# Kernel tuning notes

Measured on AMD Instinct MI355X. Metric: run time of the kernel, lower is better.

## Reference

```python
import jax, jax.numpy as jnp
import numpy as np

NUM_HEADS = 8
WINDOW = 7
DILATION = 1
EPS = 1e-5


def channel_ln(x, w, b):
    # x: [B, C, H, W]; normalize over channel dim (axis=1)
    mu = jnp.mean(x, axis=1, keepdims=True)
    var = jnp.var(x, axis=1, keepdims=True)
    xhat = (x - mu) * jax.lax.rsqrt(var + EPS)
    return xhat * w[None, :, None, None] + b[None, :, None, None]


def local_mask(H, W, window, dilation):
    r = (window // 2) * dilation
    ii, jj = jnp.meshgrid(jnp.arange(H), jnp.arange(W), indexing="ij")
    ii = ii.reshape(-1)
    jj = jj.reshape(-1)
    di = jnp.abs(ii[:, None] - ii[None, :])
    dj = jnp.abs(jj[:, None] - jj[None, :])
    m = (di <= r) & (dj <= r)
    if dilation > 1:
        m = m & (di % dilation == 0) & (dj % dilation == 0)
    return m  # [N, N] bool


def local_attention(x, qkv_w, qkv_b, proj_w, proj_b):
    B, C, H, W = x.shape
    N = H * W
    hd = C // NUM_HEADS
    t = x.reshape(B, C, N).transpose(0, 2, 1)            # [B, N, C]
    qkv = t @ qkv_w.T + qkv_b                            # [B, N, 3C]
    qkv = qkv.reshape(B, N, 3, NUM_HEADS, hd)
    q, k, v = (qkv[:, :, i].transpose(0, 2, 1, 3) for i in range(3))  # [B,h,N,d]
    scale = 1.0 / jnp.sqrt(jnp.asarray(hd, x.dtype))
    scores = jnp.einsum("bhnd,bhmd->bhnm", q, k) * scale  # [B,h,N,N]
    mask = local_mask(H, W, WINDOW, DILATION)             # [N,N]
    scores = jnp.where(mask[None, None], scores, jnp.asarray(-jnp.inf, x.dtype))
    attn = jax.nn.softmax(scores, axis=-1)
    out = jnp.einsum("bhnm,bhmd->bhnd", attn, v)          # [B,h,N,d]
    out = out.transpose(0, 2, 1, 3).reshape(B, N, C)      # [B,N,C]
    out = out @ proj_w.T + proj_b
    return out.transpose(0, 2, 1).reshape(B, C, H, W)


def mlp2d(x, fc1_w, fc1_b, fc2_w, fc2_b):
    # 1x1 convs == per-pixel linear over channels
    h = jnp.einsum("bchw,oc->bohw", x, fc1_w) + fc1_b[None, :, None, None]
    h = jax.nn.gelu(h, approximate=False)
    return jnp.einsum("bchw,oc->bohw", h, fc2_w) + fc2_b[None, :, None, None]


def setup_inputs() -> dict:
    key = jax.random.key(0)
    ks = jax.random.split(key, 12)
    B, C, H, W = 1, 256, 56, 56
    hidden = 4 * C
    s = lambda fan: 1.0 / np.sqrt(fan)
    return {
        "x": jax.random.normal(ks[0], (B, C, H, W), jnp.float32),
        "norm1_w": jnp.ones((C,), jnp.float32),
        "norm1_b": jnp.zeros((C,), jnp.float32),
        "qkv_w": jax.random.normal(ks[1], (3 * C, C), jnp.float32) * s(C),
        "qkv_b": jnp.zeros((3 * C,), jnp.float32),
        "proj_w": jax.random.normal(ks[2], (C, C), jnp.float32) * s(C),
        "proj_b": jnp.zeros((C,), jnp.float32),
        "norm2_w": jnp.ones((C,), jnp.float32),
        "norm2_b": jnp.zeros((C,), jnp.float32),
        "fc1_w": jax.random.normal(ks[3], (hidden, C), jnp.float32) * s(C),
        "fc1_b": jnp.zeros((hidden,), jnp.float32),
        "fc2_w": jax.random.normal(ks[4], (C, hidden), jnp.float32) * s(hidden),
        "fc2_b": jnp.zeros((C,), jnp.float32),
    }


def reference(x, norm1_w, norm1_b, qkv_w, qkv_b, proj_w, proj_b,
              norm2_w, norm2_b, fc1_w, fc1_b, fc2_w, fc2_b):
    x = x + local_attention(channel_ln(x, norm1_w, norm1_b), qkv_w, qkv_b, proj_w, proj_b)
    x = x + mlp2d(channel_ln(x, norm2_w, norm2_b), fc1_w, fc1_b, fc2_w, fc2_b)
    return x
```

## Files before the change

kernel.cpp:

```cpp
#include <hip/hip_runtime.h>
#include <math.h>


typedef unsigned int uint;
typedef unsigned short ushort;
typedef unsigned long long u64;
typedef __attribute__((ext_vector_type(8))) short short8;
typedef __attribute__((ext_vector_type(4))) float floatx4;
typedef __attribute__((ext_vector_type(4))) unsigned short ushort4v;

#define AS1(p) (const __attribute__((address_space(1))) void*)(p)
#define AS3(p) (__attribute__((address_space(3))) void*)(p)

__device__ __forceinline__ float bf2f(ushort u) {
  union { uint i; float f; } v; v.i = ((uint)u) << 16; return v.f;
}
__device__ __forceinline__ ushort f2bf(float f) {
  union { float f; uint i; } v; v.f = f;
  uint u = v.i;
  return (ushort)((u + 0x7fffu + ((u >> 16) & 1u)) >> 16);
}

__device__ __forceinline__ void stage64(const ushort* src, int kstride,
                                        ushort* dstBase, int tid) {
  const int srow = tid >> 5;
  const int scb  = (tid & 31) ^ srow;
  const ushort* g = src + (size_t)srow * kstride + scb * 8;
  ushort* d = dstBase + tid * 8;
  #pragma unroll
  for (int r = 0; r < 8; ++r) {
    __builtin_amdgcn_global_load_lds(AS1(g), AS3(d), 16, 0, 0);
    g += 8 * kstride;
    d += 2048;
  }
}

__device__ __forceinline__ void compute64(const ushort* As, const ushort* Bs,
                                          int w, int lane, floatx4 acc[4]) {
  const int fm = lane & 15;
  const int q  = lane >> 4;
  const int swz = fm & 7;
  const int arow = (w * 16 + fm) * 256;
  #pragma unroll
  for (int kt = 0; kt < 8; ++kt) {
    const int blk = ((kt * 4 + q) ^ swz) * 8;
    short8 af = *(const short8*)&As[arow + blk];
    #pragma unroll
    for (int nt = 0; nt < 4; ++nt) {
      short8 bfr = *(const short8*)&Bs[(nt * 16 + fm) * 256 + blk];
      acc[nt] = __builtin_amdgcn_mfma_f32_16x16x32_bf16(af, bfr, acc[nt], 0, 0, 0);
    }
  }
}

__global__ __launch_bounds__(256) void prep_kernel(
    const float* __restrict__ x, const float* __restrict__ n1w,
    const float* __restrict__ n1b, const float* __restrict__ qkvw,
    ushort* __restrict__ t1, ushort* __restrict__ wcat)
{
  const int tid = threadIdx.x;
  const int bid = blockIdx.x;
  if (bid >= 196) {
    int idx = (bid - 196) * 256 + tid;
    wcat[idx] = f2bf(qkvw[idx]);
    return;
  }
  __shared__ float tile[256 * 17];
  __shared__ float red[2][16][16];
  __shared__ float mu[16], rsv[16];
  const int n0 = bid * 16;
  const int px = tid & 15, grp = tid >> 4;
  #pragma unroll 4
  for (int it = 0; it < 16; ++it) {
    int c = it * 16 + grp;
    tile[c * 17 + px] = x[(size_t)c * 3136 + n0 + px];
  }
  __syncthreads();
  float s = 0.f, ss = 0.f;
  #pragma unroll
  for (int i = 0; i < 16; ++i) {
    float v = tile[(grp * 16 + i) * 17 + px];
    s += v; ss += v * v;
  }
  red[0][px][grp] = s; red[1][px][grp] = ss;
  __syncthreads();
  if (tid < 16) {
    float s2 = 0.f, ss2 = 0.f;
    #pragma unroll
    for (int g = 0; g < 16; ++g) { s2 += red[0][tid][g]; ss2 += red[1][tid][g]; }
    float m = s2 * (1.f / 256.f);
    float var = ss2 * (1.f / 256.f) - m * m;
    mu[tid] = m;
    rsv[tid] = rsqrtf(var + 1e-5f);
  }
  __syncthreads();
  const float wc = n1w[tid], bc = n1b[tid];
  #pragma unroll 4
  for (int p = 0; p < 16; ++p) {
    float v = tile[tid * 17 + p];
    t1[(size_t)(n0 + p) * 256 + tid] = f2bf((v - mu[p]) * rsv[p] * wc + bc);
  }
}

__global__ __launch_bounds__(256, 2) void qkv_kernel(
    const ushort* __restrict__ A, const ushort* __restrict__ B,
    const float* __restrict__ bias, ushort* __restrict__ out,
    const float* __restrict__ projw, const float* __restrict__ f1w,
    const float* __restrict__ f2w, ushort* __restrict__ wcat)
{
  const int tid = threadIdx.x;
  if (blockIdx.y >= 49) {
    int c = (blockIdx.y - 49) * 12 + blockIdx.x;
    int idx = c * 256 + tid;
    float v;
    if (idx < 65536)        v = projw[idx];
    else if (idx < 327680)  v = f1w[idx - 65536];
    else                    v = f2w[idx - 327680];
    wcat[196608 + idx] = f2bf(v);
    return;
  }
  __shared__ ushort As[16384], Bs[16384];
  const int lane = tid & 63, w = tid >> 6;
  const int m0 = blockIdx.y * 64, n0 = blockIdx.x * 64;
  floatx4 acc[4] = {{0.f,0.f,0.f,0.f},{0.f,0.f,0.f,0.f},
                    {0.f,0.f,0.f,0.f},{0.f,0.f,0.f,0.f}};
  stage64(A + (size_t)m0 * 256, 256, As, tid);
  stage64(B + (size_t)n0 * 256, 256, Bs, tid);
  asm volatile("s_waitcnt vmcnt(0)" ::: "memory");
  __syncthreads();
  compute64(As, Bs, w, lane, acc);
  const int fm = lane & 15, q4 = (lane >> 4) * 4;
  #pragma unroll
  for (int nt = 0; nt < 4; ++nt)
    #pragma unroll
    for (int r = 0; r < 4; ++r) {
      int m = m0 + w * 16 + q4 + r;
      int n = n0 + nt * 16 + fm;
      float v = acc[nt][r] + bias[n];
      if (n < 256) v *= 0.17677669529663687f;
      out[(size_t)m * 768 + n] = f2bf(v);
    }
}

#define AM_SMEM 145952

__global__ __launch_bounds__(512, 1) void attnmlp_kernel(
    const ushort* __restrict__ qkv, const ushort* __restrict__ pw_bf,
    const float* __restrict__ projb, const float* __restrict__ x,
    const ushort* __restrict__ f1_bf, const float* __restrict__ f1b,
    const ushort* __restrict__ f2_bf, const float* __restrict__ f2b,
    const float* __restrict__ n2w, const float* __restrict__ n2b,
    float* __restrict__ outf)
{
  __shared__ __align__(16) char smem[AM_SMEM];
  ushort* Kh    = (ushort*)smem;
  ushort* Vh    = (ushort*)(smem + 52000);
  float*  pr    = (float*)(smem + 103200);
  ushort* aas   = (ushort*)(smem + 137504);
  ushort* pslab = (ushort*)smem;
  float*  x1s   = (float*)(smem + 103200);
  ushort* hbuf  = (ushort*)smem;
  ushort* fslab = (ushort*)(smem + 32768);
  ushort* t2s   = (ushort*)(smem + 120096);
  float*  pstat = (float*)(smem + 128288);
  float*  stats = (float*)(smem + 129312);

  const int tid = threadIdx.x;
  const int wv = tid >> 6, lane = tid & 63;
  const int fm = lane & 15, q = lane >> 4;
  const int l4 = lane >> 2, lb = lane & 3;
  const int i0 = (blockIdx.x / 14) * 4, j0 = (blockIdx.x % 14) * 4;

  for (int s = tid; s < 3200; s += 512) {
    int p = s >> 5, ck = s & 31;
    int ii = i0 - 3 + p / 10, jj = j0 - 3 + p % 10;
    if (ii >= 0 && ii < 56 && jj >= 0 && jj < 56) {
      const ushort* kr = qkv + (size_t)(ii * 56 + jj) * 768 + 256 + ck * 8;
      short8 kv = *(const short8*)kr;
      u64 lo = ((const u64*)&kv)[0], hi = ((const u64*)&kv)[1];
      *(u64*)&Kh[p * 260 + ck * 8] = lo;
      *(u64*)&Kh[p * 260 + ck * 8 + 4] = hi;
      *(short8*)&Vh[p * 256 + ck * 8] = *(const short8*)(kr + 256);
    } else {
      *(u64*)&Kh[p * 260 + ck * 8] = 0ull;
      *(u64*)&Kh[p * 260 + ck * 8 + 4] = 0ull;
      short8 z = {0, 0, 0, 0, 0, 0, 0, 0};
      *(short8*)&Vh[p * 256 + ck * 8] = z;
    }
  }
  __syncthreads();

  {
    const int h = lane >> 3, mg = lane & 7;
    #pragma unroll
    for (int qq = 0; qq < 2; ++qq) {
      const int p = wv * 2 + qq;
      const int qi = p >> 2, qj = p & 3;
      const int iq = i0 + qi, jq = j0 + qj;
      const ushort* qp = qkv + (size_t)(iq * 56 + jq) * 768 + h * 32;
      float qf[32];
      #pragma unroll
      for (int u = 0; u < 4; ++u) {
        short8 qv = *(const short8*)(qp + u * 8);
        #pragma unroll
        for (int e = 0; e < 8; ++e) qf[u * 8 + e] = bf2f((ushort)qv[e]);
      }
      float sv[7];
      float mx = -1e30f;
      #pragma unroll
      for (int k = 0; k < 7; ++k) {
        int m = mg + 8 * k;
        float s = -1e30f;
        if (m < 49) {
          int mi = m / 7, mj = m % 7;
          int ii = iq + mi - 3, jj = jq + mj - 3;
          if (ii >= 0 && ii < 56 && jj >= 0 && jj < 56) {
            int hrow = (qi + mi) * 10 + (qj + mj);
            const u64* k8 = (const u64*)&Kh[hrow * 260 + h * 32];
            float a = 0.f;
            #pragma unroll
            for (int u = 0; u < 8; ++u) {
              u64 kv = k8[u];
              #pragma unroll
              for (int e = 0; e < 4; ++e)
                a += qf[u * 4 + e] * bf2f((ushort)(kv >> (16 * e)));
            }
            s = a;
          }
        }
        sv[k] = s;
        mx = fmaxf(mx, s);
      }
      mx = fmaxf(mx, __shfl_xor(mx, 1));
      mx = fmaxf(mx, __shfl_xor(mx, 2));
      mx = fmaxf(mx, __shfl_xor(mx, 4));
      float sm = 0.f;
      #pragma unroll
      for (int k = 0; k < 7; ++k) { sv[k] = __expf(sv[k] - mx); sm += sv[k]; }
      sm += __shfl_xor(sm, 1);
      sm += __shfl_xor(sm, 2);
      sm += __shfl_xor(sm, 4);
      float inv = 1.f / sm;
      #pragma unroll
      for (int k = 0; k < 7; ++k) {
        int m = mg + 8 * k;
        pr[(p * 8 + h) * 67 + m] = sv[k] * inv;
      }
    }
  }
  __syncthreads();

  ushort* ps0 = pslab + wv * 2048;
  ushort* ps1 = ps0 + 1024;
#define STAGE_P(kt, buf) do { \
    _Pragma("unroll") \
    for (int i_ = 0; i_ < 2; ++i_) { \
      int row_ = i_ * 16 + l4; \
      const ushort* g_ = pw_bf + (size_t)(wv * 32 + row_) * 256 + (kt) * 32 + (lb ^ (row_ & 3)) * 8; \
      __builtin_amdgcn_global_load_lds(AS1(g_), AS3((buf) + i_ * 512 + lane * 8), 16, 0, 0); \
    } } while (0)
  STAGE_P(0, ps0);

  {
    const int p = tid >> 5, cg = tid & 31, hh = cg >> 2;
    const int qi = p >> 2, qj = p & 3;
    float acc8[8] = {0, 0, 0, 0, 0, 0, 0, 0};
    #pragma unroll
    for (int mi = 0; mi < 7; ++mi)
      #pragma unroll
      for (int mj = 0; mj < 7; ++mj) {
        int m = mi * 7 + mj;
        int hrow = (qi + mi) * 10 + (qj + mj);
        float pm = pr[(p * 8 + hh) * 67 + m];
        short8 v8 = *(const short8*)&Vh[hrow * 256 + cg * 8];
        #pragma unroll
        for (int e = 0; e < 8; ++e)
          acc8[e] += pm * bf2f((ushort)v8[e]);
      }
    short8 o;
    #pragma unroll
    for (int e = 0; e < 8; ++e) o[e] = (short)f2bf(acc8[e]);
    *(short8*)&aas[p * 264 + cg * 8] = o;
  }
  __syncthreads();

  {
    floatx4 pacc[2] = {{0.f,0.f,0.f,0.f},{0.f,0.f,0.f,0.f}};
    for (int kt = 0; kt < 8; ++kt) {
      ushort* cur = (kt & 1) ? ps1 : ps0;
      ushort* nxt = (kt & 1) ? ps0 : ps1;
      if (kt < 7) {
        STAGE_P(kt + 1, nxt);
        asm volatile("s_waitcnt vmcnt(2)" ::: "memory");
      } else {
        asm volatile("s_waitcnt vmcnt(0)" ::: "memory");
      }
      short8 af = *(const short8*)&aas[fm * 264 + kt * 32 + q * 8];
      #pragma unroll
      for (int nt = 0; nt < 2; ++nt) {
        int r = nt * 16 + fm;
        short8 bfr = *(const short8*)&cur[r * 32 + (q ^ (r & 3)) * 8];
        pacc[nt] = __builtin_amdgcn_mfma_f32_16x16x32_bf16(af, bfr, pacc[nt], 0, 0, 0);
      }
    }
    #pragma unroll
    for (int nt = 0; nt < 2; ++nt) {
      int ch = wv * 32 + nt * 16 + fm;
      floatx4 rx = *(const floatx4*)(x + (size_t)ch * 3136 + (i0 + q) * 56 + j0);
      #pragma unroll
      for (int r = 0; r < 4; ++r) {
        int px = q * 4 + r;
        x1s[px * 264 + ch] = pacc[nt][r] + projb[ch] + rx[r];
      }
    }
  }
  ushort* fs0 = fslab + wv * 4096;
  ushort* fs1 = fs0 + 2048;
#define STAGE_F1(c, kt, buf) do { \
    _Pragma("unroll") \
    for (int i_ = 0; i_ < 4; ++i_) { \
      int row_ = i_ * 16 + l4; \
      const ushort* g_ = f1_bf + (size_t)((c) * 64 + row_) * 256 + (kt) * 32 + (lb ^ (row_ & 3)) * 8; \
      __builtin_amdgcn_global_load_lds(AS1(g_), AS3((buf) + i_ * 512 + lane * 8), 16, 0, 0); \
    } } while (0)
  STAGE_F1(wv, 0, fs0);
  __syncthreads();

  floatx4 xv[2];
  xv[0] = *(const floatx4*)&x1s[fm * 264 + wv * 32 + q * 4];
  xv[1] = *(const floatx4*)&x1s[fm * 264 + wv * 32 + 16 + q * 4];
  {
    float s = 0.f, ss = 0.f;
    #pragma unroll
    for (int nt = 0; nt < 2; ++nt)
      #pragma unroll
      for (int e = 0; e < 4; ++e) { s += xv[nt][e]; ss += xv[nt][e] * xv[nt][e]; }
    s += __shfl_xor(s, 16); ss += __shfl_xor(ss, 16);
    s += __shfl_xor(s, 32); ss += __shfl_xor(ss, 32);
    if (lane < 16) { pstat[(wv * 16 + lane) * 2] = s; pstat[(wv * 16 + lane) * 2 + 1] = ss; }
  }
  __syncthreads();
  if (tid < 16) {
    float s2 = 0.f, ss2 = 0.f;
    #pragma unroll
    for (int ww = 0; ww < 8; ++ww) {
      s2 += pstat[(ww * 16 + tid) * 2];
      ss2 += pstat[(ww * 16 + tid) * 2 + 1];
    }
    float mu = s2 * (1.f / 256.f);
    float var = ss2 * (1.f / 256.f) - mu * mu;
    stats[tid * 2] = mu;
    stats[tid * 2 + 1] = rsqrtf(var + 1e-5f);
  }
  __syncthreads();
  {
    float mu = stats[fm * 2], rs = stats[fm * 2 + 1];
    #pragma unroll
    for (int nt = 0; nt < 2; ++nt) {
      int ch0 = wv * 32 + nt * 16 + q * 4;
      ushort4v o;
      #pragma unroll
      for (int e = 0; e < 4; ++e)
        o[e] = f2bf((xv[nt][e] - mu) * rs * n2w[ch0 + e] + n2b[ch0 + e]);
      int slot = ch0 >> 3;
      *(ushort4v*)&t2s[fm * 256 + ((slot ^ (fm & 7)) * 8) + (ch0 & 7)] = o;
    }
  }
  float f1br[2][4];
  #pragma unroll
  for (int ci = 0; ci < 2; ++ci)
    #pragma unroll
    for (int nt = 0; nt < 4; ++nt)
      f1br[ci][nt] = f1b[(wv + ci * 8) * 64 + nt * 16 + fm];
  __syncthreads();

  {
    floatx4 fa[4] = {{0.f,0.f,0.f,0.f},{0.f,0.f,0.f,0.f},
                     {0.f,0.f,0.f,0.f},{0.f,0.f,0.f,0.f}};
    for (int sidx = 0; sidx < 16; ++sidx) {
      const int kt = sidx & 7;
      const int ci = sidx >> 3;
      ushort* cur = (sidx & 1) ? fs1 : fs0;
      ushort* nxt = (sidx & 1) ? fs0 : fs1;
      if (sidx < 15) {
        int s1 = sidx + 1;
        STAGE_F1(wv + (s1 >> 3) * 8, s1 & 7, nxt);
        asm volatile("s_waitcnt vmcnt(4)" ::: "memory");
      } else {
        asm volatile("s_waitcnt vmcnt(0)" ::: "memory");
      }
      short8 af = *(const short8*)&t2s[fm * 256 + (((kt * 4 + q) ^ (fm & 7)) * 8)];
      #pragma unroll
      for (int nt = 0; nt < 4; ++nt) {
        int r = nt * 16 + fm;
        short8 bfr = *(const short8*)&cur[r * 32 + (q ^ (r & 3)) * 8];
        fa[nt] = __builtin_amdgcn_mfma_f32_16x16x32_bf16(af, bfr, fa[nt], 0, 0, 0);
      }
      if (kt == 7) {
        #pragma unroll
        for (int nt = 0; nt < 4; ++nt) {
          int hc = (wv + ci * 8) * 64 + nt * 16 + fm;
          #pragma unroll
          for (int r4 = 0; r4 < 4; ++r4) {
            int prow = q * 4 + r4;
            float v = fa[nt][r4] + f1br[ci][nt];
            v = 0.5f * v * (1.0f + erff(v * 0.70710678118654752f));
            hbuf[prow * 1024 + (((hc >> 3) ^ (prow & 7)) * 8) + (hc & 7)] = f2bf(v);
            fa[nt][r4] = 0.f;
          }
        }
      }
    }
  }
  ushort* gs3[3] = {fs0, fs0 + 1024, fs0 + 2048};
#define STAGE_F2(kt, buf) do { \
    _Pragma("unroll") \
    for (int i_ = 0; i_ < 2; ++i_) { \
      int row_ = i_ * 16 + l4; \
      const ushort* g_ = f2_bf + (size_t)(wv * 32 + row_) * 1024 + (kt) * 32 + (lb ^ (row_ & 3)) * 8; \
      __builtin_amdgcn_global_load_lds(AS1(g_), AS3((buf) + i_ * 512 + lane * 8), 16, 0, 0); \
    } } while (0)
  STAGE_F2(0, gs3[0]);
  STAGE_F2(1, gs3[1]);
  __syncthreads();

  {
    floatx4 ga[2] = {{0.f,0.f,0.f,0.f},{0.f,0.f,0.f,0.f}};
    for (int kt = 0; kt < 32; ++kt) {
      if (kt < 30) {
        STAGE_F2(kt + 2, gs3[(kt + 2) % 3]);
        asm volatile("s_waitcnt vmcnt(4)" ::: "memory");
      } else if (kt == 30) {
        asm volatile("s_waitcnt vmcnt(0)" ::: "memory");
      }
      ushort* cur = gs3[kt % 3];
      short8 bfr = *(const short8*)&hbuf[fm * 1024 + (((kt * 4 + q) ^ (fm & 7)) * 8)];
      #pragma unroll
      for (int mt = 0; mt < 2; ++mt) {
        int r = mt * 16 + fm;
        short8 af = *(const short8*)&cur[r * 32 + (q ^ (r & 3)) * 8];
        ga[mt] = __builtin_amdgcn_mfma_f32_16x16x32_bf16(af, bfr, ga[mt], 0, 0, 0);
      }
    }
    #pragma unroll
    for (int mt = 0; mt < 2; ++mt) {
      #pragma unroll
      for (int r4 = 0; r4 < 4; ++r4) {
        int ch = wv * 32 + mt * 16 + q * 4 + r4;
        int n = (i0 + (fm >> 2)) * 56 + j0 + (fm & 3);
        outf[(size_t)ch * 3136 + n] = ga[mt][r4] + f2b[ch] + xv[mt][r4];
      }
    }
  }
#undef STAGE_P
#undef STAGE_F1
#undef STAGE_F2
}

extern "C" void kernel_launch(void* const* d_in, const int* in_sizes, int n_in,
                              void* d_out, int out_size, void* d_ws, size_t ws_size,
                              hipStream_t stream) {
  const float* x     = (const float*)d_in[0];
  const float* n1w   = (const float*)d_in[1];
  const float* n1b   = (const float*)d_in[2];
  const float* qkvw  = (const float*)d_in[3];
  const float* qkvb  = (const float*)d_in[4];
  const float* projw = (const float*)d_in[5];
  const float* projb = (const float*)d_in[6];
  const float* n2w   = (const float*)d_in[7];
  const float* n2b   = (const float*)d_in[8];
  const float* f1w   = (const float*)d_in[9];
  const float* f1b   = (const float*)d_in[10];
  const float* f2w   = (const float*)d_in[11];
  const float* f2b   = (const float*)d_in[12];

  char* ws = (char*)d_ws;
  ushort* wcat = (ushort*)(ws + 0);
  ushort* t    = (ushort*)(ws + 4784128);
  ushort* qh   = (ushort*)(ws + 6389760);

  const ushort* qw_bf = wcat;
  const ushort* pw_bf = wcat + 196608;
  const ushort* f1_bf = wcat + 262144;
  const ushort* f2_bf = wcat + 524288;
  float* outf = (float*)d_out;

  hipLaunchKernelGGL(prep_kernel, dim3(964), dim3(256), 0, stream,
                     x, n1w, n1b, qkvw, t, wcat);
  hipLaunchKernelGGL(qkv_kernel, dim3(12, 241), dim3(256), 0, stream,
                     t, qw_bf, qkvb, qh, projw, f1w, f2w, wcat);
  hipLaunchKernelGGL(attnmlp_kernel, dim3(196), dim3(512), 0, stream,
                     qh, pw_bf, projb, x, f1_bf, f1b, f2_bf, f2b,
                     n2w, n2b, outf);
}
```

Measured before the change: 125.5 us.

## Double attention-MLP block to 1024 threads, halving per-wave work

The fused attention+MLP kernel now launches 1024 threads (16 waves) per block instead of 512. Each wave handles one query pixel in the score phase, 4 channels in the PV phase, and 16 output channels in the proj/fc2 GEMMs and 32-column chunks in fc1. Staging loads and waitcnt depths are halved to match, and the stat buffers move to a slightly larger shared-memory region. The aim is more latency hiding per CU with only 196 blocks. The cost is fewer MFMAs per wave between LDS reads, a tighter register budget, and more barrier participants.

Result: faster. 122.7 us (-2.2%).

```diff
diff --git a/kernel.cpp b/kernel.cpp
--- a/kernel.cpp
+++ b/kernel.cpp
@@ -142,9 +142,9 @@
     }
 }
 
-#define AM_SMEM 145952
-
-__global__ __launch_bounds__(512, 1) void attnmlp_kernel(
+#define AM_SMEM 148128
+
+__global__ __launch_bounds__(1024, 1) void attnmlp_kernel(
     const ushort* __restrict__ qkv, const ushort* __restrict__ pw_bf,
     const float* __restrict__ projb, const float* __restrict__ x,
     const ushort* __restrict__ f1_bf, const float* __restrict__ f1b,
@@ -162,8 +162,8 @@
   ushort* hbuf  = (ushort*)smem;
   ushort* fslab = (ushort*)(smem + 32768);
   ushort* t2s   = (ushort*)(smem + 120096);
-  float*  pstat = (float*)(smem + 128288);
-  float*  stats = (float*)(smem + 129312);
+  float*  pstat = (float*)(smem + 145952);
+  float*  stats = (float*)(smem + 148000);
 
   const int tid = threadIdx.x;
   const int wv = tid >> 6, lane = tid & 63;
@@ -171,7 +171,7 @@
   const int l4 = lane >> 2, lb = lane & 3;
   const int i0 = (blockIdx.x / 14) * 4, j0 = (blockIdx.x % 14) * 4;
 
-  for (int s = tid; s < 3200; s += 512) {
+  for (int s = tid; s < 3200; s += 1024) {
     int p = s >> 5, ck = s & 31;
     int ii = i0 - 3 + p / 10, jj = j0 - 3 + p % 10;
     if (ii >= 0 && ii < 56 && jj >= 0 && jj < 56) {
@@ -192,79 +192,73 @@
 
   {
     const int h = lane >> 3, mg = lane & 7;
-    #pragma unroll
-    for (int qq = 0; qq < 2; ++qq) {
-      const int p = wv * 2 + qq;
-      const int qi = p >> 2, qj = p & 3;
-      const int iq = i0 + qi, jq = j0 + qj;
-      const ushort* qp = qkv + (size_t)(iq * 56 + jq) * 768 + h * 32;
-      float qf[32];
+    const int p = wv;
+    const int qi = p >> 2, qj = p & 3;
+    const int iq = i0 + qi, jq = j0 + qj;
+    const ushort* qp = qkv + (size_t)(iq * 56 + jq) * 768 + h * 32;
+    float qf[32];
+    #pragma unroll
+    for (int u = 0; u < 4; ++u) {
+      short8 qv = *(const short8*)(qp + u * 8);
       #pragma unroll
-      for (int u = 0; u < 4; ++u) {
-        short8 qv = *(const short8*)(qp + u * 8);
-        #pragma unroll
-        for (int e = 0; e < 8; ++e) qf[u * 8 + e] = bf2f((ushort)qv[e]);
-      }
-      float sv[7];
-      float mx = -1e30f;
-      #pragma unroll
-      for (int k = 0; k < 7; ++k) {
-        int m = mg + 8 * k;
-        float s = -1e30f;
-        if (m < 49) {
-          int mi = m / 7, mj = m % 7;
-          int ii = iq + mi - 3, jj = jq + mj - 3;
-          if (ii >= 0 && ii < 56 && jj >= 0 && jj < 56) {
-            int hrow = (qi + mi) * 10 + (qj + mj);
-            const u64* k8 = (const u64*)&Kh[hrow * 260 + h * 32];
-            float a = 0.f;
+      for (int e = 0; e < 8; ++e) qf[u * 8 + e] = bf2f((ushort)qv[e]);
+    }
+    float sv[7];
+    float mx = -1e30f;
+    #pragma unroll
+    for (int k = 0; k < 7; ++k) {
+      int m = mg + 8 * k;
+      float s = -1e30f;
+      if (m < 49) {
+        int mi = m / 7, mj = m % 7;
+        int ii = iq + mi - 3, jj = jq + mj - 3;
+        if (ii >= 0 && ii < 56 && jj >= 0 && jj < 56) {
+          int hrow = (qi + mi) * 10 + (qj + mj);
+          const u64* k8 = (const u64*)&Kh[hrow * 260 + h * 32];
+          float a = 0.f;
+          #pragma unroll
+          for (int u = 0; u < 8; ++u) {
+            u64 kv = k8[u];
             #pragma unroll
-            for (int u = 0; u < 8; ++u) {
-              u64 kv = k8[u];
-              #pragma unroll
-              for (int e = 0; e < 4; ++e)
-                a += qf[u * 4 + e] * bf2f((ushort)(kv >> (16 * e)));
-            }
-            s = a;
+            for (int e = 0; e < 4; ++e)
+              a += qf[u * 4 + e] * bf2f((ushort)(kv >> (16 * e)));
           }
+          s = a;
         }
-        sv[k] = s;
-        mx = fmaxf(mx, s);
-      }
-      mx = fmaxf(mx, __shfl_xor(mx, 1));
-      mx = fmaxf(mx, __shfl_xor(mx, 2));
-      mx = fmaxf(mx, __shfl_xor(mx, 4));
-      float sm = 0.f;
-      #pragma unroll
-      for (int k = 0; k < 7; ++k) { sv[k] = __expf(sv[k] - mx); sm += sv[k]; }
-      sm += __shfl_xor(sm, 1);
-      sm += __shfl_xor(sm, 2);
-      sm += __shfl_xor(sm, 4);
-      float inv = 1.f / sm;
-      #pragma unroll
-      for (int k = 0; k < 7; ++k) {
-        int m = mg + 8 * k;
-        pr[(p * 8 + h) * 67 + m] = sv[k] * inv;
-      }
-    }
-  }
-  __syncthreads();
-
-  ushort* ps0 = pslab + wv * 2048;
-  ushort* ps1 = ps0 + 1024;
+      }
+      sv[k] = s;
+      mx = fmaxf(mx, s);
+    }
+    mx = fmaxf(mx, __shfl_xor(mx, 1));
+    mx = fmaxf(mx, __shfl_xor(mx, 2));
+    mx = fmaxf(mx, __shfl_xor(mx, 4));
+    float sm = 0.f;
+    #pragma unroll
+    for (int k = 0; k < 7; ++k) { sv[k] = __expf(sv[k] - mx); sm += sv[k]; }
+    sm += __shfl_xor(sm, 1);
+    sm += __shfl_xor(sm, 2);
+    sm += __shfl_xor(sm, 4);
+    float inv = 1.f / sm;
+    #pragma unroll
+    for (int k = 0; k < 7; ++k) {
+      int m = mg + 8 * k;
+      pr[(p * 8 + h) * 67 + m] = sv[k] * inv;
+    }
+  }
+  __syncthreads();
+
+  ushort* ps0 = pslab + wv * 1024;
+  ushort* ps1 = ps0 + 512;
 #define STAGE_P(kt, buf) do { \
-    _Pragma("unroll") \
-    for (int i_ = 0; i_ < 2; ++i_) { \
-      int row_ = i_ * 16 + l4; \
-      const ushort* g_ = pw_bf + (size_t)(wv * 32 + row_) * 256 + (kt) * 32 + (lb ^ (row_ & 3)) * 8; \
-      __builtin_amdgcn_global_load_lds(AS1(g_), AS3((buf) + i_ * 512 + lane * 8), 16, 0, 0); \
-    } } while (0)
+    const ushort* g_ = pw_bf + (size_t)(wv * 16 + l4) * 256 + (kt) * 32 + (lb ^ (l4 & 3)) * 8; \
+    __builtin_amdgcn_global_load_lds(AS1(g_), AS3((buf) + lane * 8), 16, 0, 0); \
+  } while (0)
   STAGE_P(0, ps0);
 
   {
-    const int p = tid >> 5, cg = tid & 31, hh = cg >> 2;
+    const int p = tid >> 6, c4 = tid & 63, hh = c4 >> 3;
     const int qi = p >> 2, qj = p & 3;
-    float acc8[8] = {0, 0, 0, 0, 0, 0, 0, 0};
+    float acc4[4] = {0, 0, 0, 0};
     #pragma unroll
     for (int mi = 0; mi < 7; ++mi)
       #pragma unroll
@@ -272,69 +266,57 @@
         int m = mi * 7 + mj;
         int hrow = (qi + mi) * 10 + (qj + mj);
         float pm = pr[(p * 8 + hh) * 67 + m];
-        short8 v8 = *(const short8*)&Vh[hrow * 256 + cg * 8];
+        u64 v4 = *(const u64*)&Vh[hrow * 256 + c4 * 4];
         #pragma unroll
-        for (int e = 0; e < 8; ++e)
-          acc8[e] += pm * bf2f((ushort)v8[e]);
-      }
-    short8 o;
-    #pragma unroll
-    for (int e = 0; e < 8; ++e) o[e] = (short)f2bf(acc8[e]);
-    *(short8*)&aas[p * 264 + cg * 8] = o;
-  }
-  __syncthreads();
-
-  {
-    floatx4 pacc[2] = {{0.f,0.f,0.f,0.f},{0.f,0.f,0.f,0.f}};
+        for (int e = 0; e < 4; ++e)
+          acc4[e] += pm * bf2f((ushort)(v4 >> (16 * e)));
+      }
+    ushort4v o;
+    #pragma unroll
+    for (int e = 0; e < 4; ++e) o[e] = f2bf(acc4[e]);
+    *(ushort4v*)&aas[p * 264 + c4 * 4] = o;
+  }
+  __syncthreads();
+
+  {
+    floatx4 pacc = {0.f, 0.f, 0.f, 0.f};
     for (int kt = 0; kt < 8; ++kt) {
       ushort* cur = (kt & 1) ? ps1 : ps0;
       ushort* nxt = (kt & 1) ? ps0 : ps1;
       if (kt < 7) {
         STAGE_P(kt + 1, nxt);
-        asm volatile("s_waitcnt vmcnt(2)" ::: "memory");
+        asm volatile("s_waitcnt vmcnt(1)" ::: "memory");
       } else {
         asm volatile("s_waitcnt vmcnt(0)" ::: "memory");
       }
       short8 af = *(const short8*)&aas[fm * 264 + kt * 32 + q * 8];
-      #pragma unroll
-      for (int nt = 0; nt < 2; ++nt) {
-        int r = nt * 16 + fm;
-        short8 bfr = *(const short8*)&cur[r * 32 + (q ^ (r & 3)) * 8];
-        pacc[nt] = __builtin_amdgcn_mfma_f32_16x16x32_bf16(af, bfr, pacc[nt], 0, 0, 0);
-      }
-    }
-    #pragma unroll
-    for (int nt = 0; nt < 2; ++nt) {
-      int ch = wv * 32 + nt * 16 + fm;
-      floatx4 rx = *(const floatx4*)(x + (size_t)ch * 3136 + (i0 + q) * 56 + j0);
-      #pragma unroll
-      for (int r = 0; r < 4; ++r) {
-        int px = q * 4 + r;
-        x1s[px * 264 + ch] = pacc[nt][r] + projb[ch] + rx[r];
-      }
-    }
-  }
-  ushort* fs0 = fslab + wv * 4096;
-  ushort* fs1 = fs0 + 2048;
+      short8 bfr = *(const short8*)&cur[fm * 32 + ((q ^ (fm & 3)) * 8)];
+      pacc = __builtin_amdgcn_mfma_f32_16x16x32_bf16(af, bfr, pacc, 0, 0, 0);
+    }
+    int ch = wv * 16 + fm;
+    floatx4 rx = *(const floatx4*)(x + (size_t)ch * 3136 + (i0 + q) * 56 + j0);
+    #pragma unroll
+    for (int r = 0; r < 4; ++r) {
+      int px = q * 4 + r;
+      x1s[px * 264 + ch] = pacc[r] + projb[ch] + rx[r];
+    }
+  }
+  ushort* fs0 = fslab + wv * 2048;
+  ushort* fs1 = fs0 + 1024;
 #define STAGE_F1(c, kt, buf) do { \
     _Pragma("unroll") \
-    for (int i_ = 0; i_ < 4; ++i_) { \
+    for (int i_ = 0; i_ < 2; ++i_) { \
       int row_ = i_ * 16 + l4; \
-      const ushort* g_ = f1_bf + (size_t)((c) * 64 + row_) * 256 + (kt) * 32 + (lb ^ (row_ & 3)) * 8; \
+      const ushort* g_ = f1_bf + (size_t)((c) * 32 + row_) * 256 + (kt) * 32 + (lb ^ (row_ & 3)) * 8; \
       __builtin_amdgcn_global_load_lds(AS1(g_), AS3((buf) + i_ * 512 + lane * 8), 16, 0, 0); \
     } } while (0)
   STAGE_F1(wv, 0, fs0);
   __syncthreads();
 
-  floatx4 xv[2];
-  xv[0] = *(const floatx4*)&x1s[fm * 264 + wv * 32 + q * 4];
-  xv[1] = *(const floatx4*)&x1s[fm * 264 + wv * 32 + 16 + q * 4];
-  {
-    float s = 0.f, ss = 0.f;
-    #pragma unroll
-    for (int nt = 0; nt < 2; ++nt)
-      #pragma unroll
-      for (int e = 0; e < 4; ++e) { s += xv[nt][e]; ss += xv[nt][e] * xv[nt][e]; }
+  floatx4 xv = *(const floatx4*)&x1s[fm * 264 + wv * 16 + q * 4];
+  {
+    float s = xv[0] + xv[1] + xv[2] + xv[3];
+    float ss = xv[0]*xv[0] + xv[1]*xv[1] + xv[2]*xv[2] + xv[3]*xv[3];
     s += __shfl_xor(s, 16); ss += __shfl_xor(ss, 16);
     s += __shfl_xor(s, 32); ss += __shfl_xor(ss, 32);
     if (lane < 16) { pstat[(wv * 16 + lane) * 2] = s; pstat[(wv * 16 + lane) * 2 + 1] = ss; }
@@ -343,7 +325,7 @@
   if (tid < 16) {
     float s2 = 0.f, ss2 = 0.f;
     #pragma unroll
-    for (int ww = 0; ww < 8; ++ww) {
+    for (int ww = 0; ww < 16; ++ww) {
       s2 += pstat[(ww * 16 + tid) * 2];
       ss2 += pstat[(ww * 16 + tid) * 2 + 1];
     }
@@ -355,28 +337,24 @@
   __syncthreads();
   {
     float mu = stats[fm * 2], rs = stats[fm * 2 + 1];
-    #pragma unroll
-    for (int nt = 0; nt < 2; ++nt) {
-      int ch0 = wv * 32 + nt * 16 + q * 4;
-      ushort4v o;
-      #pragma unroll
-      for (int e = 0; e < 4; ++e)
-        o[e] = f2bf((xv[nt][e] - mu) * rs * n2w[ch0 + e] + n2b[ch0 + e]);
-      int slot = ch0 >> 3;
-      *(ushort4v*)&t2s[fm * 256 + ((slot ^ (fm & 7)) * 8) + (ch0 & 7)] = o;
-    }
-  }
-  float f1br[2][4];
+    int ch0 = wv * 16 + q * 4;
+    ushort4v o;
+    #pragma unroll
+    for (int e = 0; e < 4; ++e)
+      o[e] = f2bf((xv[e] - mu) * rs * n2w[ch0 + e] + n2b[ch0 + e]);
+    int slot = ch0 >> 3;
+    *(ushort4v*)&t2s[fm * 256 + ((slot ^ (fm & 7)) * 8) + (ch0 & 7)] = o;
+  }
+  float f1br[2][2];
   #pragma unroll
   for (int ci = 0; ci < 2; ++ci)
     #pragma unroll
-    for (int nt = 0; nt < 4; ++nt)
-      f1br[ci][nt] = f1b[(wv + ci * 8) * 64 + nt * 16 + fm];
-  __syncthreads();
-
-  {
-    floatx4 fa[4] = {{0.f,0.f,0.f,0.f},{0.f,0.f,0.f,0.f},
-                     {0.f,0.f,0.f,0.f},{0.f,0.f,0.f,0.f}};
+    for (int nt = 0; nt < 2; ++nt)
+      f1br[ci][nt] = f1b[(wv + ci * 16) * 32 + nt * 16 + fm];
+  __syncthreads();
+
+  {
+    floatx4 fa[2] = {{0.f,0.f,0.f,0.f},{0.f,0.f,0.f,0.f}};
     for (int sidx = 0; sidx < 16; ++sidx) {
       const int kt = sidx & 7;
       const int ci = sidx >> 3;
@@ -384,22 +362,22 @@
       ushort* nxt = (sidx & 1) ? fs0 : fs1;
       if (sidx < 15) {
         int s1 = sidx + 1;
-        STAGE_F1(wv + (s1 >> 3) * 8, s1 & 7, nxt);
-        asm volatile("s_waitcnt vmcnt(4)" ::: "memory");
+        STAGE_F1(wv + (s1 >> 3) * 16, s1 & 7, nxt);
+        asm volatile("s_waitcnt vmcnt(2)" ::: "memory");
       } else {
         asm volatile("s_waitcnt vmcnt(0)" ::: "memory");
       }
       short8 af = *(const short8*)&t2s[fm * 256 + (((kt * 4 + q) ^ (fm & 7)) * 8)];
       #pragma unroll
-      for (int nt = 0; nt < 4; ++nt) {
+      for (int nt = 0; nt < 2; ++nt) {
         int r = nt * 16 + fm;
         short8 bfr = *(const short8*)&cur[r * 32 + (q ^ (r & 3)) * 8];
         fa[nt] = __builtin_amdgcn_mfma_f32_16x16x32_bf16(af, bfr, fa[nt], 0, 0, 0);
       }
       if (kt == 7) {
         #pragma unroll
-        for (int nt = 0; nt < 4; ++nt) {
-          int hc = (wv + ci * 8) * 64 + nt * 16 + fm;
+        for (int nt = 0; nt < 2; ++nt) {
+          int hc = (wv + ci * 16) * 32 + nt * 16 + fm;
           #pragma unroll
           for (int r4 = 0; r4 < 4; ++r4) {
             int prow = q * 4 + r4;
@@ -412,44 +390,34 @@
       }
     }
   }
-  ushort* gs3[3] = {fs0, fs0 + 1024, fs0 + 2048};
+  ushort* gs3[3] = {fs0, fs0 + 512, fs0 + 1024};
 #define STAGE_F2(kt, buf) do { \
-    _Pragma("unroll") \
-    for (int i_ = 0; i_ < 2; ++i_) { \
-      int row_ = i_ * 16 + l4; \
-      const ushort* g_ = f2_bf + (size_t)(wv * 32 + row_) * 1024 + (kt) * 32 + (lb ^ (row_ & 3)) * 8; \
-      __builtin_amdgcn_global_load_lds(AS1(g_), AS3((buf) + i_ * 512 + lane * 8), 16, 0, 0); \
-    } } while (0)
+    const ushort* g_ = f2_bf + (size_t)(wv * 16 + l4) * 1024 + (kt) * 32 + (lb ^ (l4 & 3)) * 8; \
+    __builtin_amdgcn_global_load_lds(AS1(g_), AS3((buf) + lane * 8), 16, 0, 0); \
+  } while (0)
   STAGE_F2(0, gs3[0]);
   STAGE_F2(1, gs3[1]);
   __syncthreads();
 
   {
-    floatx4 ga[2] = {{0.f,0.f,0.f,0.f},{0.f,0.f,0.f,0.f}};
+    floatx4 ga = {0.f, 0.f, 0.f, 0.f};
     for (int kt = 0; kt < 32; ++kt) {
       if (kt < 30) {
         STAGE_F2(kt + 2, gs3[(kt + 2) % 3]);
-        asm volatile("s_waitcnt vmcnt(4)" ::: "memory");
+        asm volatile("s_waitcnt vmcnt(2)" ::: "memory");
       } else if (kt == 30) {
         asm volatile("s_waitcnt vmcnt(0)" ::: "memory");
       }
       ushort* cur = gs3[kt % 3];
+      short8 af = *(const short8*)&cur[fm * 32 + ((q ^ (fm & 3)) * 8)];
       short8 bfr = *(const short8*)&hbuf[fm * 1024 + (((kt * 4 + q) ^ (fm & 7)) * 8)];
-      #pragma unroll
-      for (int mt = 0; mt < 2; ++mt) {
-        int r = mt * 16 + fm;
-        short8 af = *(const short8*)&cur[r * 32 + (q ^ (r & 3)) * 8];
-        ga[mt] = __builtin_amdgcn_mfma_f32_16x16x32_bf16(af, bfr, ga[mt], 0, 0, 0);
-      }
-    }
-    #pragma unroll
-    for (int mt = 0; mt < 2; ++mt) {
-      #pragma unroll
-      for (int r4 = 0; r4 < 4; ++r4) {
-        int ch = wv * 32 + mt * 16 + q * 4 + r4;
-        int n = (i0 + (fm >> 2)) * 56 + j0 + (fm & 3);
-        outf[(size_t)ch * 3136 + n] = ga[mt][r4] + f2b[ch] + xv[mt][r4];
-      }
+      ga = __builtin_amdgcn_mfma_f32_16x16x32_bf16(af, bfr, ga, 0, 0, 0);
+    }
+    #pragma unroll
+    for (int r4 = 0; r4 < 4; ++r4) {
+      int ch = wv * 16 + q * 4 + r4;
+      int n = (i0 + (fm >> 2)) * 56 + j0 + (fm & 3);
+      outf[(size_t)ch * 3136 + n] = ga[r4] + f2b[ch] + xv[r4];
     }
   }
 #undef STAGE_P
@@ -489,7 +457,7 @@
                      x, n1w, n1b, qkvw, t, wcat);
   hipLaunchKernelGGL(qkv_kernel, dim3(12, 241), dim3(256), 0, stream,
                      t, qw_bf, qkvb, qh, projw, f1w, f2w, wcat);
-  hipLaunchKernelGGL(attnmlp_kernel, dim3(196), dim3(512), 0, stream,
+  hipLaunchKernelGGL(attnmlp_kernel, dim3(196), dim3(1024), 0, stream,
                      qh, pw_bf, projb, x, f1_bf, f1b, f2_bf, f2b,
                      n2w, n2b, outf);
 }
```
